# Kernel optimization log

Measured on AMD Instinct MI355X. Metric: run time of the kernel, lower is better.

## Reference

```python
import jax, jax.numpy as jnp
import numpy as np

D = 1024            # text/user embedding length
HID = 3 * D         # 2*text_D + user_D = MLP hidden width
OUT = 8             # output_shape (int)


def setup_inputs() -> dict:
    key = jax.random.key(0)
    ks = jax.random.split(key, 9)
    T, U = 256, 128
    s = 1.0 / np.sqrt(HID)
    return {
        "text_a": jax.random.normal(ks[0], (T, D), jnp.float32),
        "text_b": jax.random.normal(ks[1], (T, D), jnp.float32),
        "user_embeddings": jax.random.normal(ks[2], (U, D), jnp.float32),
        "W1": jax.random.uniform(ks[3], (HID, HID), jnp.float32, -s, s),
        "b1": jax.random.uniform(ks[4], (HID,), jnp.float32, -s, s),
        "W2": jax.random.uniform(ks[5], (HID, HID), jnp.float32, -s, s),
        "b2": jax.random.uniform(ks[6], (HID,), jnp.float32, -s, s),
        "W3": jax.random.uniform(ks[7], (OUT, HID), jnp.float32, -s, s),
        "b3": jax.random.uniform(ks[8], (OUT,), jnp.float32, -s, s),
    }


def reference(text_a, text_b, user_embeddings, W1, b1, W2, b2, W3, b3):
    # min/max over the set of text embedding tensors
    t_min = jnp.minimum(text_a, text_b)          # (T, D)
    t_max = jnp.maximum(text_a, text_b)          # (T, D)
    T, U = t_min.shape[0], user_embeddings.shape[0]
    # combined[t, u] = concat(t_min[t], t_max[t], user[u])  -> (T, U, 3D)
    text_part = jnp.broadcast_to(
        jnp.concatenate([t_min, t_max], axis=-1)[:, None, :], (T, U, 2 * D))
    user_part = jnp.broadcast_to(user_embeddings[None, :, :], (T, U, D))
    x = jnp.concatenate([text_part, user_part], axis=-1)  # (T, U, 3D)
    # 3-layer MLP (no activation, no dropout by default)
    x = jnp.einsum('tuh,oh->tuo', x, W1) + b1
    x = jnp.einsum('tuh,oh->tuo', x, W2) + b2
    x = jnp.einsum('tuh,oh->tuo', x, W3) + b3
    return x  # (T, U, OUT)
```

## Files before the change

kernel.cpp:

```cpp
#include <hip/hip_runtime.h>
#include <hip/hip_bf16.h>


#define HIDN 3072
#define DIM 1024
#define NOUT 8
#define NS 32
#define KPS 96
#define RPT 12
#define GX 24
#define CPB 128
#define TDIM 256
#define UDIM 128
#define PF4 6144

__device__ __forceinline__ float4 f4z() { return make_float4(0.f, 0.f, 0.f, 0.f); }
__device__ __forceinline__ float4 add4(float4 a, float4 b) {
    return make_float4(a.x + b.x, a.y + b.y, a.z + b.z, a.w + b.w);
}
__device__ __forceinline__ float dot4(float4 a, float4 b) {
    return a.x * b.x + a.y * b.y + a.z * b.z + a.w * b.w;
}

__device__ __forceinline__ void bias_slice_fold(const float* As,
                                                const float* __restrict__ bvec,
                                                float* __restrict__ cp,
                                                int s, int tid) {
    const int o = tid >> 5, k5 = tid & 31;
    float acc = 0.f;
#pragma unroll
    for (int j = 0; j < KPS / 32; ++j)
        acc += As[o * KPS + k5 + 32 * j] * bvec[s * KPS + k5 + 32 * j];
#pragma unroll
    for (int off = 16; off; off >>= 1) acc += __shfl_down(acc, off, 32);
    if (k5 == 0) cp[s * NOUT + o] = acc;
}

__global__ __launch_bounds__(256) void gemm_partial(
    const float* __restrict__ A_rows, const float* __restrict__ part_in,
    const float* __restrict__ B, float* __restrict__ part_out,
    const float* __restrict__ bvec, float* __restrict__ cp, int mode) {
    const int s = blockIdx.y, gx = blockIdx.x;
    const int tid = threadIdx.x;
    const int rq = tid >> 5, c4 = tid & 31;

    __shared__ float As[NOUT * KPS];
    __shared__ float4 red[8 * NOUT * 32];

    const int k0 = s * KPS + rq * RPT;
    const float4* Bp = (const float4*)(B + (size_t)k0 * HIDN) + gx * 32 + c4;
    float4 bv[RPT];
#pragma unroll
    for (int kk = 0; kk < RPT; ++kk) bv[kk] = Bp[(size_t)kk * (HIDN / 4)];

    if (mode == 0) {
        for (int i = tid; i < NOUT * KPS; i += 256)
            As[i] = A_rows[(i / KPS) * HIDN + s * KPS + (i % KPS)];
    } else {
        if (tid < NOUT * KPS / 4) {
            const int j4 = tid;
            const int o = j4 / (KPS / 4), kk4 = j4 % (KPS / 4);
            const float4* pp = (const float4*)(part_in + (size_t)o * HIDN
                                               + s * KPS) + kk4;
            float4 a = f4z();
#pragma unroll 16
            for (int sp = 0; sp < NS; ++sp)
                a = add4(a, pp[(size_t)sp * PF4]);
            ((float4*)As)[j4] = a;
        }
    }
    __syncthreads();
    if (gx == 0) bias_slice_fold(As, bvec, cp, s, tid);

    float4 acc[NOUT];
#pragma unroll
    for (int o = 0; o < NOUT; ++o) acc[o] = f4z();
#pragma unroll
    for (int kk = 0; kk < RPT; ++kk) {
#pragma unroll
        for (int o = 0; o < NOUT; ++o) {
            float a = As[o * KPS + rq * RPT + kk];
            acc[o].x += a * bv[kk].x; acc[o].y += a * bv[kk].y;
            acc[o].z += a * bv[kk].z; acc[o].w += a * bv[kk].w;
        }
    }

#pragma unroll
    for (int o = 0; o < NOUT; ++o) red[rq * 256 + o * 32 + c4] = acc[o];
    __syncthreads();
    {
        const int o = tid >> 5, cc = tid & 31;
        float4 r = f4z();
#pragma unroll
        for (int q = 0; q < 8; ++q) r = add4(r, red[q * 256 + o * 32 + cc]);
        *(float4*)(part_out + ((size_t)s * NOUT + o) * HIDN + gx * CPB + cc * 4) = r;
    }
}

__global__ __launch_bounds__(256) void k3_mid(
    const float* __restrict__ part2, const float* __restrict__ user,
    float* __restrict__ Mt, float* __restrict__ Qpart) {
    const int b = blockIdx.x, tid = threadIdx.x;
    const float4* p4 = (const float4*)part2;

    if (b < 128) {
        const int li = tid & 31, sg = tid >> 5;
        const int i4 = b * 32 + li;
        const int o = i4 >> 9, h4 = i4 & 511;
        float4 acc = f4z();
#pragma unroll
        for (int j = 0; j < 4; ++j)
            acc = add4(acc, p4[(size_t)(sg * 4 + j) * PF4 + o * 768 + h4]);
        __shared__ float4 red2[8 * 32];
        red2[sg * 32 + li] = acc;
        __syncthreads();
        if (tid < 32) {
            const int i4w = b * 32 + tid;
            float4 r = f4z();
#pragma unroll
            for (int q = 0; q < 8; ++q) r = add4(r, red2[q * 32 + tid]);
            ((float4*)Mt)[i4w] = r;
        }
        return;
    }

    const int ub = b - 128;
    __shared__ float4 mup[4 * 64];
    __shared__ float4 Mu4[NOUT * 8];
    const int tgt = tid & 63, grp = tid >> 6;
    const int o = tgt >> 3, j4 = tgt & 7;
    float4 a = f4z();
#pragma unroll
    for (int j = 0; j < 8; ++j)
        a = add4(a, p4[(size_t)(grp * 8 + j) * PF4 + o * 768 + 512 + ub * 8 + j4]);
    mup[grp * 64 + tgt] = a;
    __syncthreads();
    if (tid < 64)
        Mu4[tid] = add4(add4(mup[tid], mup[64 + tid]),
                        add4(mup[128 + tid], mup[192 + tid]));
    __syncthreads();

    const int u = tid >> 1, o0 = (tid & 1) * 4;
    const float4* uv = (const float4*)user + (size_t)u * (DIM / 4) + ub * 8;
    float4 x8[8];
#pragma unroll
    for (int j = 0; j < 8; ++j) x8[j] = uv[j];
    float q[4];
#pragma unroll
    for (int oo = 0; oo < 4; ++oo) {
        float s = 0.f;
#pragma unroll
        for (int j = 0; j < 8; ++j) s += dot4(Mu4[(o0 + oo) * 8 + j], x8[j]);
        q[oo] = s;
    }
    ((float4*)Qpart)[((size_t)ub * UDIM + u) * 2 + (tid & 1)] =
        make_float4(q[0], q[1], q[2], q[3]);
}

__global__ __launch_bounds__(256) void k4_out(
    const float* __restrict__ ta, const float* __restrict__ tb,
    const float* __restrict__ Mt, const float* __restrict__ Qpart,
    const float* __restrict__ cp1, const float* __restrict__ cp2,
    const float* __restrict__ b3, float4* __restrict__ out) {
    const int t = blockIdx.x, tid = threadIdx.x;
    const int lane = tid & 63, w = tid >> 6;

    const float4* Mt4 = (const float4*)Mt;
    float4 a = ((const float4*)ta)[(size_t)t * (DIM / 4) + tid];
    float4 b = ((const float4*)tb)[(size_t)t * (DIM / 4) + tid];
    float4 mn = make_float4(fminf(a.x, b.x), fminf(a.y, b.y),
                            fminf(a.z, b.z), fminf(a.w, b.w));
    float4 mx = make_float4(fmaxf(a.x, b.x), fmaxf(a.y, b.y),
                            fmaxf(a.z, b.z), fmaxf(a.w, b.w));
    float acc[NOUT];
#pragma unroll
    for (int o = 0; o < NOUT; ++o) {
        float4 ml = Mt4[o * 512 + tid];
        float4 mh = Mt4[o * 512 + 256 + tid];
        acc[o] = dot4(ml, mn) + dot4(mh, mx);
    }
#pragma unroll
    for (int o = 0; o < NOUT; ++o) {
#pragma unroll
        for (int off = 32; off > 0; off >>= 1)
            acc[o] += __shfl_down(acc[o], off, 64);
    }
    __shared__ float red[4][NOUT];
    __shared__ float c8[NOUT];
    if (lane == 0) {
#pragma unroll
        for (int o = 0; o < NOUT; ++o) red[w][o] = acc[o];
    }
    if (tid < NOUT) {
        float cc = b3[tid];
#pragma unroll 8
        for (int s = 0; s < NS; ++s)
            cc += cp1[s * NOUT + tid] + cp2[s * NOUT + tid];
        c8[tid] = cc;
    }
    __syncthreads();

    const int u = tid >> 1, half = tid & 1, o0 = half * 4;
    const float4* Qp4 = (const float4*)Qpart;
    float4 q = f4z();
#pragma unroll 8
    for (int ub = 0; ub < 32; ++ub)
        q = add4(q, Qp4[((size_t)ub * UDIM + u) * 2 + half]);

    float4 cv = make_float4(c8[o0], c8[o0 + 1], c8[o0 + 2], c8[o0 + 3]);
    float4 pv = make_float4(
        red[0][o0 + 0] + red[1][o0 + 0] + red[2][o0 + 0] + red[3][o0 + 0],
        red[0][o0 + 1] + red[1][o0 + 1] + red[2][o0 + 1] + red[3][o0 + 1],
        red[0][o0 + 2] + red[1][o0 + 2] + red[2][o0 + 2] + red[3][o0 + 2],
        red[0][o0 + 3] + red[1][o0 + 3] + red[2][o0 + 3] + red[3][o0 + 3]);
    out[(size_t)t * 256 + tid] = add4(add4(pv, q), cv);
}

extern "C" void kernel_launch(void* const* d_in, const int* in_sizes, int n_in,
                              void* d_out, int out_size, void* d_ws, size_t ws_size,
                              hipStream_t stream) {
    const float* text_a = (const float*)d_in[0];
    const float* text_b = (const float*)d_in[1];
    const float* user   = (const float*)d_in[2];
    const float* W1 = (const float*)d_in[3];
    const float* b1 = (const float*)d_in[4];
    const float* W2 = (const float*)d_in[5];
    const float* b2 = (const float*)d_in[6];
    const float* W3 = (const float*)d_in[7];
    const float* b3 = (const float*)d_in[8];

    float* ws = (float*)d_ws;
    float* part1 = ws;
    float* part2 = part1 + (size_t)NS * NOUT * HIDN;
    float* Mt    = part2 + (size_t)NS * NOUT * HIDN;
    float* Qpart = Mt + NOUT * 2048;
    float* cp1   = Qpart + 32 * UDIM * NOUT;
    float* cp2   = cp1 + NS * NOUT;

    gemm_partial<<<dim3(GX, NS), 256, 0, stream>>>(W3, nullptr, W2, part1,
                                                   b2, cp2, 0);
    gemm_partial<<<dim3(GX, NS), 256, 0, stream>>>(nullptr, part1, W1, part2,
                                                   b1, cp1, 1);
    k3_mid<<<160, 256, 0, stream>>>(part2, user, Mt, Qpart);
    k4_out<<<TDIM, 256, 0, stream>>>(text_a, text_b, Mt, Qpart, cp1, cp2, b3,
                                     (float4*)d_out);
}
```

Before: 36.40 us.

## Fuse mid-stage reduction into second GEMM via atomic-counter tail blocks

Removes the separate k3_mid launch. The last 160 blocks of the second gemm_partial take a ticket from a global atomic counter, spin until all 768 blocks have finished, then do the Mt/Qpart reductions. The B-tile register loads are moved after the A staging, and the unroll factor of the partial-sum loop is reduced. This saves one kernel launch and its gap, but adds a spin-wait that assumes every block is co-resident or gets scheduled, and it puts atomic traffic on the critical path.

Measured after the change: 87.51 us. 2.4x slower.

```diff
diff --git a/kernel.cpp b/kernel.cpp
--- a/kernel.cpp
+++ b/kernel.cpp
@@ -13,6 +13,9 @@
 #define TDIM 256
 #define UDIM 128
 #define PF4 6144
+#define NBLK2 768
+#define NTAIL 160
+#define TAIL0 (NBLK2 - NTAIL)
 
 __device__ __forceinline__ float4 f4z() { return make_float4(0.f, 0.f, 0.f, 0.f); }
 __device__ __forceinline__ float4 add4(float4 a, float4 b) {
@@ -36,10 +39,68 @@
     if (k5 == 0) cp[s * NOUT + o] = acc;
 }
 
+__device__ __forceinline__ void tail_mt(const float4* __restrict__ p4,
+                                        float* __restrict__ Mt,
+                                        int b, int tid, float4* redls) {
+    const int li = tid & 31, sg = tid >> 5;
+    const int i4 = b * 32 + li;
+    const int o = i4 >> 9, h4 = i4 & 511;
+    float4 acc = f4z();
+#pragma unroll
+    for (int j = 0; j < 4; ++j)
+        acc = add4(acc, p4[(size_t)(sg * 4 + j) * PF4 + o * 768 + h4]);
+    redls[sg * 32 + li] = acc;
+    __syncthreads();
+    if (tid < 32) {
+        float4 r = f4z();
+#pragma unroll
+        for (int q = 0; q < 8; ++q) r = add4(r, redls[q * 32 + tid]);
+        ((float4*)Mt)[b * 32 + tid] = r;
+    }
+}
+
+__device__ __forceinline__ void tail_q(const float4* __restrict__ p4,
+                                       const float* __restrict__ user,
+                                       float* __restrict__ Qpart,
+                                       int ub, int tid, float4* redls) {
+    float4* mup = redls;
+    float4* Mu4 = redls + 256;
+    const int tgt = tid & 63, grp = tid >> 6;
+    const int o = tgt >> 3, j4 = tgt & 7;
+    float4 a = f4z();
+#pragma unroll
+    for (int j = 0; j < 8; ++j)
+        a = add4(a, p4[(size_t)(grp * 8 + j) * PF4 + o * 768 + 512 + ub * 8 + j4]);
+    mup[grp * 64 + tgt] = a;
+    __syncthreads();
+    if (tid < 64)
+        Mu4[tid] = add4(add4(mup[tid], mup[64 + tid]),
+                        add4(mup[128 + tid], mup[192 + tid]));
+    __syncthreads();
+
+    const int u = tid >> 1, o0 = (tid & 1) * 4;
+    const float4* uv = (const float4*)user + (size_t)u * (DIM / 4) + ub * 8;
+    float4 x8[8];
+#pragma unroll
+    for (int j = 0; j < 8; ++j) x8[j] = uv[j];
+    float q[4];
+#pragma unroll
+    for (int oo = 0; oo < 4; ++oo) {
+        float s = 0.f;
+#pragma unroll
+        for (int j = 0; j < 8; ++j) s += dot4(Mu4[(o0 + oo) * 8 + j], x8[j]);
+        q[oo] = s;
+    }
+    ((float4*)Qpart)[((size_t)ub * UDIM + u) * 2 + (tid & 1)] =
+        make_float4(q[0], q[1], q[2], q[3]);
+}
+
 __global__ __launch_bounds__(256) void gemm_partial(
     const float* __restrict__ A_rows, const float* __restrict__ part_in,
     const float* __restrict__ B, float* __restrict__ part_out,
-    const float* __restrict__ bvec, float* __restrict__ cp, int mode) {
+    const float* __restrict__ bvec, float* __restrict__ cp,
+    const float* __restrict__ user, float* __restrict__ Mt,
+    float* __restrict__ Qpart, int* __restrict__ ctr, int mode) {
     const int s = blockIdx.y, gx = blockIdx.x;
     const int tid = threadIdx.x;
     const int rq = tid >> 5, c4 = tid & 31;
@@ -47,13 +108,8 @@
     __shared__ float As[NOUT * KPS];
     __shared__ float4 red[8 * NOUT * 32];
 
-    const int k0 = s * KPS + rq * RPT;
-    const float4* Bp = (const float4*)(B + (size_t)k0 * HIDN) + gx * 32 + c4;
-    float4 bv[RPT];
-#pragma unroll
-    for (int kk = 0; kk < RPT; ++kk) bv[kk] = Bp[(size_t)kk * (HIDN / 4)];
-
     if (mode == 0) {
+        if (s == 0 && gx == 0 && tid == 0) *ctr = 0;
         for (int i = tid; i < NOUT * KPS; i += 256)
             As[i] = A_rows[(i / KPS) * HIDN + s * KPS + (i % KPS)];
     } else {
@@ -63,7 +119,7 @@
             const float4* pp = (const float4*)(part_in + (size_t)o * HIDN
                                                + s * KPS) + kk4;
             float4 a = f4z();
-#pragma unroll 16
+#pragma unroll 8
             for (int sp = 0; sp < NS; ++sp)
                 a = add4(a, pp[(size_t)sp * PF4]);
             ((float4*)As)[j4] = a;
@@ -71,6 +127,13 @@
     }
     __syncthreads();
     if (gx == 0) bias_slice_fold(As, bvec, cp, s, tid);
+
+    const int k0 = s * KPS + rq * RPT;
+    const float4* Bp = (const float4*)(B + (size_t)k0 * HIDN) + gx * 32 + c4;
+
+    float4 bv[RPT];
+#pragma unroll
+    for (int kk = 0; kk < RPT; ++kk) bv[kk] = Bp[(size_t)kk * (HIDN / 4)];
 
     float4 acc[NOUT];
 #pragma unroll
@@ -95,66 +158,29 @@
         for (int q = 0; q < 8; ++q) r = add4(r, red[q * 256 + o * 32 + cc]);
         *(float4*)(part_out + ((size_t)s * NOUT + o) * HIDN + gx * CPB + cc * 4) = r;
     }
-}
-
-__global__ __launch_bounds__(256) void k3_mid(
-    const float* __restrict__ part2, const float* __restrict__ user,
-    float* __restrict__ Mt, float* __restrict__ Qpart) {
-    const int b = blockIdx.x, tid = threadIdx.x;
-    const float4* p4 = (const float4*)part2;
-
-    if (b < 128) {
-        const int li = tid & 31, sg = tid >> 5;
-        const int i4 = b * 32 + li;
-        const int o = i4 >> 9, h4 = i4 & 511;
-        float4 acc = f4z();
-#pragma unroll
-        for (int j = 0; j < 4; ++j)
-            acc = add4(acc, p4[(size_t)(sg * 4 + j) * PF4 + o * 768 + h4]);
-        __shared__ float4 red2[8 * 32];
-        red2[sg * 32 + li] = acc;
-        __syncthreads();
-        if (tid < 32) {
-            const int i4w = b * 32 + tid;
-            float4 r = f4z();
-#pragma unroll
-            for (int q = 0; q < 8; ++q) r = add4(r, red2[q * 32 + tid]);
-            ((float4*)Mt)[i4w] = r;
+
+    if (mode == 0) return;
+
+    __shared__ int item_s;
+    __syncthreads();
+    if (tid == 0) {
+        int old = __hip_atomic_fetch_add(ctr, 1, __ATOMIC_ACQ_REL,
+                                         __HIP_MEMORY_SCOPE_AGENT);
+        int item = old - TAIL0;
+        if (item >= 0) {
+            while (__hip_atomic_load(ctr, __ATOMIC_ACQUIRE,
+                                     __HIP_MEMORY_SCOPE_AGENT) < NBLK2) { }
         }
-        return;
-    }
-
-    const int ub = b - 128;
-    __shared__ float4 mup[4 * 64];
-    __shared__ float4 Mu4[NOUT * 8];
-    const int tgt = tid & 63, grp = tid >> 6;
-    const int o = tgt >> 3, j4 = tgt & 7;
-    float4 a = f4z();
-#pragma unroll
-    for (int j = 0; j < 8; ++j)
-        a = add4(a, p4[(size_t)(grp * 8 + j) * PF4 + o * 768 + 512 + ub * 8 + j4]);
-    mup[grp * 64 + tgt] = a;
-    __syncthreads();
-    if (tid < 64)
-        Mu4[tid] = add4(add4(mup[tid], mup[64 + tid]),
-                        add4(mup[128 + tid], mup[192 + tid]));
-    __syncthreads();
-
-    const int u = tid >> 1, o0 = (tid & 1) * 4;
-    const float4* uv = (const float4*)user + (size_t)u * (DIM / 4) + ub * 8;
-    float4 x8[8];
-#pragma unroll
-    for (int j = 0; j < 8; ++j) x8[j] = uv[j];
-    float q[4];
-#pragma unroll
-    for (int oo = 0; oo < 4; ++oo) {
-        float s = 0.f;
-#pragma unroll
-        for (int j = 0; j < 8; ++j) s += dot4(Mu4[(o0 + oo) * 8 + j], x8[j]);
-        q[oo] = s;
-    }
-    ((float4*)Qpart)[((size_t)ub * UDIM + u) * 2 + (tid & 1)] =
-        make_float4(q[0], q[1], q[2], q[3]);
+        item_s = item;
+    }
+    __syncthreads();
+    const int item = item_s;
+    if (item < 0) return;
+    __threadfence();
+
+    const float4* p4 = (const float4*)part_out;
+    if (item < 128) tail_mt(p4, Mt, item, tid, red);
+    else           tail_q(p4, user, Qpart, item - 128, tid, red);
 }
 
 __global__ __launch_bounds__(256) void k4_out(
@@ -236,12 +262,14 @@
     float* Qpart = Mt + NOUT * 2048;
     float* cp1   = Qpart + 32 * UDIM * NOUT;
     float* cp2   = cp1 + NS * NOUT;
+    int*   ctr   = (int*)(cp2 + NS * NOUT);
 
     gemm_partial<<<dim3(GX, NS), 256, 0, stream>>>(W3, nullptr, W2, part1,
-                                                   b2, cp2, 0);
+                                                   b2, cp2, user, Mt, Qpart,
+                                                   ctr, 0);
     gemm_partial<<<dim3(GX, NS), 256, 0, stream>>>(nullptr, part1, W1, part2,
-                                                   b1, cp1, 1);
-    k3_mid<<<160, 256, 0, stream>>>(part2, user, Mt, Qpart);
+                                                   b1, cp1, user, Mt, Qpart,
+                                                   ctr, 1);
     k4_out<<<TDIM, 256, 0, stream>>>(text_a, text_b, Mt, Qpart, cp1, cp2, b3,
                                      (float4*)d_out);
 }
```
